# Kernel tuning notes

Measured on AMD Instinct MI355X. Metric: run time of the kernel, lower is better.

## Reference

```python
import jax, jax.numpy as jnp
import numpy as np

B, LQ, LK = 4, 256, 512
DQ = DK = PROJ = 256


def setup_inputs() -> dict:
    key = jax.random.key(0)
    ks = jax.random.split(key, 8)
    query = jax.random.normal(ks[0], (B, LQ, DQ), dtype=jnp.float32)
    keys = jax.random.normal(ks[1], (B, LK, DK), dtype=jnp.float32)
    attn_mask = jax.random.bernoulli(ks[2], 0.1, (B, LQ, LK))
    # Linear(query_size+key_size, proj) split into query/key halves (same math as concat @ W1)
    s1 = 1.0 / np.sqrt(DQ + DK)
    Wq = jax.random.uniform(ks[3], (DQ, PROJ), jnp.float32, -s1, s1)
    Wk = jax.random.uniform(ks[4], (DK, PROJ), jnp.float32, -s1, s1)
    b1 = jax.random.uniform(ks[5], (PROJ,), jnp.float32, -s1, s1)
    s2 = 1.0 / np.sqrt(PROJ)
    w2 = jax.random.uniform(ks[6], (PROJ,), jnp.float32, -s2, s2)
    b2 = jax.random.uniform(ks[7], (), jnp.float32, -s2, s2)
    return {"query": query, "keys": keys, "attn_mask": attn_mask,
            "Wq": Wq, "Wk": Wk, "b1": b1, "w2": w2, "b2": b2}


def reference(query, keys, attn_mask, Wq, Wk, b1, w2, b2):
    # cat(q_expand, k_expand) @ W1 == q@Wq broadcast-added to k@Wk (avoids the huge concat)
    qp = jnp.einsum('bqd,dp->bqp', query, Wq)            # (B,Lq,P)
    kp = jnp.einsum('bkd,dp->bkp', keys, Wk)             # (B,Lk,P)
    h = jnp.tanh(qp[:, :, None, :] + kp[:, None, :, :] + b1)  # (B,Lq,Lk,P)
    logits = jnp.einsum('bqkp,p->bqk', h, w2) + b2        # (B,Lq,Lk)
    logits = jnp.where(attn_mask, -jnp.inf, logits)
    return logits
```

## Files before the change

### kernel.cpp

```cpp
#include <hip/hip_runtime.h>
#include <math.h>

#define B_ 4
#define LQ_ 256
#define LK_ 512
#define D_ 256
#define P_ 256

#define SC 2.8853900817779268f

#define MASK_SENTINEL (-3.0e38f)

__global__ __launch_bounds__(128) void proj_kernel(
    const float* __restrict__ Q, const float* __restrict__ Kx,
    const float* __restrict__ Wq, const float* __restrict__ Wk,
    const float* __restrict__ b1,
    float* __restrict__ Eq, float* __restrict__ Ek)
{
    __shared__ __align__(16) float As[32][17];
    __shared__ __align__(16) float Ws[32][68];

    const int bm = blockIdx.x >> 2;
    const int bn = blockIdx.x & 3;
    const bool isq = (bm < 64);
    const int m0 = isq ? bm * 16 : (bm - 64) * 16;
    const float* A = isq ? Q : Kx;
    const float* W = isq ? Wq : Wk;
    float* outp    = isq ? Eq : Ek;
    const int n0 = bn * 64;

    const int t  = threadIdx.x;
    const int tx = t & 15;
    const int ty = t >> 4;

    float acc[2][4] = {};

    for (int kt = 0; kt < D_ / 32; ++kt) {
        const int d0 = kt * 32;
        __syncthreads();
        {
            int m  = t >> 3;
            int c4 = (t & 7) * 4;
            float4 v = *(const float4*)&A[(size_t)(m0 + m) * D_ + d0 + c4];
            As[c4 + 0][m] = v.x;
            As[c4 + 1][m] = v.y;
            As[c4 + 2][m] = v.z;
            As[c4 + 3][m] = v.w;
        }
        #pragma unroll
        for (int i = 0; i < 4; ++i) {
            int f  = t + i * 128;
            int r  = f >> 4;
            int c4 = (f & 15) * 4;
            *(float4*)&Ws[r][c4] = *(const float4*)&W[(size_t)(d0 + r) * P_ + n0 + c4];
        }
        __syncthreads();
        #pragma unroll
        for (int k = 0; k < 32; ++k) {
            float a0 = As[k][ty];
            float a1 = As[k][ty + 8];
            float4 w = *(const float4*)&Ws[k][tx * 4];
            float wv[4] = {w.x, w.y, w.z, w.w};
            #pragma unroll
            for (int j = 0; j < 4; ++j) {
                acc[0][j] = fmaf(a0, wv[j], acc[0][j]);
                acc[1][j] = fmaf(a1, wv[j], acc[1][j]);
            }
        }
    }

    float bv[4] = {0.f, 0.f, 0.f, 0.f};
    if (!isq) {
        float4 b = *(const float4*)&b1[n0 + tx * 4];
        bv[0] = b.x; bv[1] = b.y; bv[2] = b.z; bv[3] = b.w;
    }

    #pragma unroll
    for (int i = 0; i < 2; ++i) {
        int m = m0 + ty + i * 8;
        float4 o;
        o.x = __builtin_amdgcn_exp2f(SC * (acc[i][0] + bv[0]));
        o.y = __builtin_amdgcn_exp2f(SC * (acc[i][1] + bv[1]));
        o.z = __builtin_amdgcn_exp2f(SC * (acc[i][2] + bv[2]));
        o.w = __builtin_amdgcn_exp2f(SC * (acc[i][3] + bv[3]));
        *(float4*)&outp[(size_t)m * P_ + n0 + tx * 4] = o;
    }
}

__global__ __launch_bounds__(256) void logits_kernel(
    const float* __restrict__ Eq, const float* __restrict__ Ek,
    const unsigned char* __restrict__ mask,
    const float* __restrict__ w2, const float* __restrict__ b2,
    float* __restrict__ out)
{
    __shared__ __align__(16) float eqs[32][260];
    __shared__ __align__(16) float eks[32][260];
    __shared__ __align__(16) float ws2[256];
    __shared__ float partial[4];

    const int b  = blockIdx.z;
    const int q0 = blockIdx.y * 32;
    const int k0 = blockIdx.x * 32;
    const int t  = threadIdx.x;

    #pragma unroll
    for (int i = 0; i < 8; ++i) {
        int f = t + i * 256;
        int r = f >> 6;
        int c = (f & 63) * 4;
        *(float4*)&eqs[r][c] = *(const float4*)&Eq[(size_t)(b * LQ_ + q0 + r) * P_ + c];
        *(float4*)&eks[r][c] = *(const float4*)&Ek[(size_t)(b * LK_ + k0 + r) * P_ + c];
    }
    float wv = w2[t];
    ws2[t] = wv;
    #pragma unroll
    for (int s = 32; s > 0; s >>= 1) wv += __shfl_xor(wv, s);
    if ((t & 63) == 0) partial[t >> 6] = wv;
    __syncthreads();

    const float base = partial[0] + partial[1] + partial[2] + partial[3] + b2[0];

    const int tx = t & 15;
    const int ty = t >> 4;
    const float* q0p = &eqs[ty][0];
    const float* q1p = &eqs[ty + 16][0];
    const float* k0p = &eks[tx][0];
    const float* k1p = &eks[tx + 16][0];

    float a00 = 0.f, a01 = 0.f, a10 = 0.f, a11 = 0.f;

    #pragma unroll 4
    for (int p4 = 0; p4 < 64; ++p4) {
        float4 qa = *(const float4*)(q0p + p4 * 4);
        float4 qb = *(const float4*)(q1p + p4 * 4);
        float4 ka = *(const float4*)(k0p + p4 * 4);
        float4 kb = *(const float4*)(k1p + p4 * 4);
        float4 w  = *(const float4*)&ws2[p4 * 4];
        float qav[4] = {qa.x, qa.y, qa.z, qa.w};
        float qbv[4] = {qb.x, qb.y, qb.z, qb.w};
        float kav[4] = {ka.x, ka.y, ka.z, ka.w};
        float kbv[4] = {kb.x, kb.y, kb.z, kb.w};
        float wvv[4] = {w.x, w.y, w.z, w.w};
        #pragma unroll
        for (int j = 0; j < 4; ++j) {
            a00 = fmaf(wvv[j], __builtin_amdgcn_rcpf(fmaf(qav[j], kav[j], 1.f)), a00);
            a01 = fmaf(wvv[j], __builtin_amdgcn_rcpf(fmaf(qav[j], kbv[j], 1.f)), a01);
            a10 = fmaf(wvv[j], __builtin_amdgcn_rcpf(fmaf(qbv[j], kav[j], 1.f)), a10);
            a11 = fmaf(wvv[j], __builtin_amdgcn_rcpf(fmaf(qbv[j], kbv[j], 1.f)), a11);
        }
    }

    const float r00 = fmaf(-2.f, a00, base);
    const float r01 = fmaf(-2.f, a01, base);
    const float r10 = fmaf(-2.f, a10, base);
    const float r11 = fmaf(-2.f, a11, base);

    const int qa_i = q0 + ty,  qb_i = q0 + ty + 16;
    const int ka_i = k0 + tx,  kb_i = k0 + tx + 16;
    const size_t row0 = (size_t)(b * LQ_ + qa_i) * LK_;
    const size_t row1 = (size_t)(b * LQ_ + qb_i) * LK_;

    out[row0 + ka_i] = mask[row0 + ka_i] ? MASK_SENTINEL : r00;
    out[row0 + kb_i] = mask[row0 + kb_i] ? MASK_SENTINEL : r01;
    out[row1 + ka_i] = mask[row1 + ka_i] ? MASK_SENTINEL : r10;
    out[row1 + kb_i] = mask[row1 + kb_i] ? MASK_SENTINEL : r11;
}

extern "C" void kernel_launch(void* const* d_in, const int* in_sizes, int n_in,
                              void* d_out, int out_size, void* d_ws, size_t ws_size,
                              hipStream_t stream) {
    const float* query        = (const float*)d_in[0];
    const float* keys         = (const float*)d_in[1];
    const unsigned char* mask = (const unsigned char*)d_in[2];
    const float* Wq           = (const float*)d_in[3];
    const float* Wk           = (const float*)d_in[4];
    const float* b1           = (const float*)d_in[5];
    const float* w2           = (const float*)d_in[6];
    const float* b2           = (const float*)d_in[7];
    float* out = (float*)d_out;

    float* Eq = (float*)d_ws;
    float* Ek = Eq + (size_t)B_ * LQ_ * P_;

    proj_kernel<<<768, 128, 0, stream>>>(query, keys, Wq, Wk, b1, Eq, Ek);

    dim3 g2(LK_ / 32, LQ_ / 32, B_);
    logits_kernel<<<g2, 256, 0, stream>>>(Eq, Ek, mask, w2, b2, out);
}
```

Baseline: 36.51 us.

## Enlarge per-thread register tiles in projection and logits kernels

The projection kernel now uses 32-row M tiles, a 64-deep K step and a 4x4 per-thread accumulator, which halves its grid and raises register-level reuse. The logits kernel drops to 128 threads per block, each computing a 4x2 output tile, so every shared-memory float4 load feeds more rcp/FMA work. Mask bytes are prefetched before the main loop so their global latency can overlap the compute. The cost is fewer threads per block for the same 32x32 tile, which lowers occupancy and latency hiding, with more registers per thread.

```diff
diff --git a/kernel.cpp b/kernel.cpp
--- a/kernel.cpp
+++ b/kernel.cpp
@@ -17,13 +17,13 @@
     const float* __restrict__ b1,
     float* __restrict__ Eq, float* __restrict__ Ek)
 {
-    __shared__ __align__(16) float As[32][17];
-    __shared__ __align__(16) float Ws[32][68];
+    __shared__ __align__(16) float As[64][36];
+    __shared__ __align__(16) float Ws[64][68];
 
     const int bm = blockIdx.x >> 2;
     const int bn = blockIdx.x & 3;
-    const bool isq = (bm < 64);
-    const int m0 = isq ? bm * 16 : (bm - 64) * 16;
+    const bool isq = (bm < 32);
+    const int m0 = isq ? bm * 32 : (bm - 32) * 32;
     const float* A = isq ? Q : Kx;
     const float* W = isq ? Wq : Wk;
     float* outp    = isq ? Eq : Ek;
@@ -33,14 +33,16 @@
     const int tx = t & 15;
     const int ty = t >> 4;
 
-    float acc[2][4] = {};
-
-    for (int kt = 0; kt < D_ / 32; ++kt) {
-        const int d0 = kt * 32;
+    float acc[4][4] = {};
+
+    for (int kt = 0; kt < 4; ++kt) {
+        const int d0 = kt * 64;
         __syncthreads();
-        {
-            int m  = t >> 3;
-            int c4 = (t & 7) * 4;
+        #pragma unroll
+        for (int i = 0; i < 4; ++i) {
+            int f  = t + i * 128;
+            int m  = f >> 4;
+            int c4 = (f & 15) * 4;
             float4 v = *(const float4*)&A[(size_t)(m0 + m) * D_ + d0 + c4];
             As[c4 + 0][m] = v.x;
             As[c4 + 1][m] = v.y;
@@ -48,24 +50,24 @@
             As[c4 + 3][m] = v.w;
         }
         #pragma unroll
-        for (int i = 0; i < 4; ++i) {
+        for (int i = 0; i < 8; ++i) {
             int f  = t + i * 128;
             int r  = f >> 4;
             int c4 = (f & 15) * 4;
             *(float4*)&Ws[r][c4] = *(const float4*)&W[(size_t)(d0 + r) * P_ + n0 + c4];
         }
         __syncthreads();
-        #pragma unroll
-        for (int k = 0; k < 32; ++k) {
-            float a0 = As[k][ty];
-            float a1 = As[k][ty + 8];
+        #pragma unroll 8
+        for (int k = 0; k < 64; ++k) {
+            float4 a = *(const float4*)&As[k][ty * 4];
             float4 w = *(const float4*)&Ws[k][tx * 4];
+            float av[4] = {a.x, a.y, a.z, a.w};
             float wv[4] = {w.x, w.y, w.z, w.w};
             #pragma unroll
-            for (int j = 0; j < 4; ++j) {
-                acc[0][j] = fmaf(a0, wv[j], acc[0][j]);
-                acc[1][j] = fmaf(a1, wv[j], acc[1][j]);
-            }
+            for (int i = 0; i < 4; ++i)
+                #pragma unroll
+                for (int j = 0; j < 4; ++j)
+                    acc[i][j] = fmaf(av[i], wv[j], acc[i][j]);
         }
     }
 
@@ -76,8 +78,8 @@
     }
 
     #pragma unroll
-    for (int i = 0; i < 2; ++i) {
-        int m = m0 + ty + i * 8;
+    for (int i = 0; i < 4; ++i) {
+        int m = m0 + ty * 4 + i;
         float4 o;
         o.x = __builtin_amdgcn_exp2f(SC * (acc[i][0] + bv[0]));
         o.y = __builtin_amdgcn_exp2f(SC * (acc[i][1] + bv[1]));
@@ -87,7 +89,7 @@
     }
 }
 
-__global__ __launch_bounds__(256) void logits_kernel(
+__global__ __launch_bounds__(128) void logits_kernel(
     const float* __restrict__ Eq, const float* __restrict__ Ek,
     const unsigned char* __restrict__ mask,
     const float* __restrict__ w2, const float* __restrict__ b2,
@@ -96,7 +98,7 @@
     __shared__ __align__(16) float eqs[32][260];
     __shared__ __align__(16) float eks[32][260];
     __shared__ __align__(16) float ws2[256];
-    __shared__ float partial[4];
+    __shared__ float partial[2];
 
     const int b  = blockIdx.z;
     const int q0 = blockIdx.y * 32;
@@ -104,66 +106,79 @@
     const int t  = threadIdx.x;
 
     #pragma unroll
-    for (int i = 0; i < 8; ++i) {
-        int f = t + i * 256;
+    for (int i = 0; i < 16; ++i) {
+        int f = t + i * 128;
         int r = f >> 6;
         int c = (f & 63) * 4;
         *(float4*)&eqs[r][c] = *(const float4*)&Eq[(size_t)(b * LQ_ + q0 + r) * P_ + c];
         *(float4*)&eks[r][c] = *(const float4*)&Ek[(size_t)(b * LK_ + k0 + r) * P_ + c];
     }
-    float wv = w2[t];
-    ws2[t] = wv;
+    float w_lo = w2[t], w_hi = w2[t + 128];
+    ws2[t] = w_lo;
+    ws2[t + 128] = w_hi;
+    float wv = w_lo + w_hi;
     #pragma unroll
     for (int s = 32; s > 0; s >>= 1) wv += __shfl_xor(wv, s);
     if ((t & 63) == 0) partial[t >> 6] = wv;
     __syncthreads();
 
-    const float base = partial[0] + partial[1] + partial[2] + partial[3] + b2[0];
+    const float base = partial[0] + partial[1] + b2[0];
 
     const int tx = t & 15;
     const int ty = t >> 4;
-    const float* q0p = &eqs[ty][0];
-    const float* q1p = &eqs[ty + 16][0];
-    const float* k0p = &eks[tx][0];
-    const float* k1p = &eks[tx + 16][0];
-
-    float a00 = 0.f, a01 = 0.f, a10 = 0.f, a11 = 0.f;
+
+    size_t oidx[4][2];
+    unsigned char mb[4][2];
+    #pragma unroll
+    for (int i = 0; i < 4; ++i)
+        #pragma unroll
+        for (int j = 0; j < 2; ++j) {
+            oidx[i][j] = (size_t)(b * LQ_ + q0 + ty + i * 8) * LK_ + (k0 + tx + j * 16);
+            mb[i][j] = mask[oidx[i][j]];
+        }
+
+    const float* qp0 = &eqs[ty][0];
+    const float* qp1 = &eqs[ty + 8][0];
+    const float* qp2 = &eqs[ty + 16][0];
+    const float* qp3 = &eqs[ty + 24][0];
+    const float* kp0 = &eks[tx][0];
+    const float* kp1 = &eks[tx + 16][0];
+
+    float acc[4][2] = {};
 
     #pragma unroll 4
     for (int p4 = 0; p4 < 64; ++p4) {
-        float4 qa = *(const float4*)(q0p + p4 * 4);
-        float4 qb = *(const float4*)(q1p + p4 * 4);
-        float4 ka = *(const float4*)(k0p + p4 * 4);
-        float4 kb = *(const float4*)(k1p + p4 * 4);
-        float4 w  = *(const float4*)&ws2[p4 * 4];
-        float qav[4] = {qa.x, qa.y, qa.z, qa.w};
-        float qbv[4] = {qb.x, qb.y, qb.z, qb.w};
-        float kav[4] = {ka.x, ka.y, ka.z, ka.w};
-        float kbv[4] = {kb.x, kb.y, kb.z, kb.w};
-        float wvv[4] = {w.x, w.y, w.z, w.w};
-        #pragma unroll
-        for (int j = 0; j < 4; ++j) {
-            a00 = fmaf(wvv[j], __builtin_amdgcn_rcpf(fmaf(qav[j], kav[j], 1.f)), a00);
-            a01 = fmaf(wvv[j], __builtin_amdgcn_rcpf(fmaf(qav[j], kbv[j], 1.f)), a01);
-            a10 = fmaf(wvv[j], __builtin_amdgcn_rcpf(fmaf(qbv[j], kav[j], 1.f)), a10);
-            a11 = fmaf(wvv[j], __builtin_amdgcn_rcpf(fmaf(qbv[j], kbv[j], 1.f)), a11);
-        }
-    }
-
-    const float r00 = fmaf(-2.f, a00, base);
-    const float r01 = fmaf(-2.f, a01, base);
-    const float r10 = fmaf(-2.f, a10, base);
-    const float r11 = fmaf(-2.f, a11, base);
-
-    const int qa_i = q0 + ty,  qb_i = q0 + ty + 16;
-    const int ka_i = k0 + tx,  kb_i = k0 + tx + 16;
-    const size_t row0 = (size_t)(b * LQ_ + qa_i) * LK_;
-    const size_t row1 = (size_t)(b * LQ_ + qb_i) * LK_;
-
-    out[row0 + ka_i] = mask[row0 + ka_i] ? MASK_SENTINEL : r00;
-    out[row0 + kb_i] = mask[row0 + kb_i] ? MASK_SENTINEL : r01;
-    out[row1 + ka_i] = mask[row1 + ka_i] ? MASK_SENTINEL : r10;
-    out[row1 + kb_i] = mask[row1 + kb_i] ? MASK_SENTINEL : r11;
+        float4 qv[4], kv[2], w;
+        qv[0] = *(const float4*)(qp0 + p4 * 4);
+        qv[1] = *(const float4*)(qp1 + p4 * 4);
+        qv[2] = *(const float4*)(qp2 + p4 * 4);
+        qv[3] = *(const float4*)(qp3 + p4 * 4);
+        kv[0] = *(const float4*)(kp0 + p4 * 4);
+        kv[1] = *(const float4*)(kp1 + p4 * 4);
+        w     = *(const float4*)&ws2[p4 * 4];
+        float qa[4][4] = {{qv[0].x,qv[0].y,qv[0].z,qv[0].w},
+                          {qv[1].x,qv[1].y,qv[1].z,qv[1].w},
+                          {qv[2].x,qv[2].y,qv[2].z,qv[2].w},
+                          {qv[3].x,qv[3].y,qv[3].z,qv[3].w}};
+        float ka[2][4] = {{kv[0].x,kv[0].y,kv[0].z,kv[0].w},
+                          {kv[1].x,kv[1].y,kv[1].z,kv[1].w}};
+        float wa[4] = {w.x, w.y, w.z, w.w};
+        #pragma unroll
+        for (int l = 0; l < 4; ++l)
+            #pragma unroll
+            for (int i = 0; i < 4; ++i)
+                #pragma unroll
+                for (int j = 0; j < 2; ++j)
+                    acc[i][j] = fmaf(wa[l],
+                        __builtin_amdgcn_rcpf(fmaf(qa[i][l], ka[j][l], 1.f)),
+                        acc[i][j]);
+    }
+
+    #pragma unroll
+    for (int i = 0; i < 4; ++i)
+        #pragma unroll
+        for (int j = 0; j < 2; ++j)
+            out[oidx[i][j]] = mb[i][j] ? MASK_SENTINEL : fmaf(-2.f, acc[i][j], base);
 }
 
 extern "C" void kernel_launch(void* const* d_in, const int* in_sizes, int n_in,
@@ -182,8 +197,8 @@
     float* Eq = (float*)d_ws;
     float* Ek = Eq + (size_t)B_ * LQ_ * P_;
 
-    proj_kernel<<<768, 128, 0, stream>>>(query, keys, Wq, Wk, b1, Eq, Ek);
+    proj_kernel<<<384, 128, 0, stream>>>(query, keys, Wq, Wk, b1, Eq, Ek);
 
     dim3 g2(LK_ / 32, LQ_ / 32, B_);
-    logits_kernel<<<g2, 256, 0, stream>>>(Eq, Ek, mask, w2, b2, out);
+    logits_kernel<<<g2, 128, 0, stream>>>(Eq, Ek, mask, w2, b2, out);
 }
```

New measurement: 41.73 us. +14.3%, slower.
